# Kernel optimization log

Measured on AMD Instinct MI355X. Metric: run time of the kernel, lower is better.

## Reference

```python
import jax, jax.numpy as jnp
import numpy as np

BATCH = 32768
NJETS = 10
NCOMBOS = 22
FF = 200
NSEL = 6
EPS = 1e-5
METRIC = jnp.array([1.0, -1.0, -1.0, -1.0], dtype=jnp.float32)  # (E,px,py,pz) Minkowski


def _cola(v, w_combo):
    # v: [b, n, 4]; w_combo: [c, n] -> [b, n+c, 4] (identity rows + learned combos)
    combos = jnp.einsum('cj,bjv->bcv', w_combo, v)
    return jnp.concatenate([v, combos], axis=1)


def _lola(v, w_e, w_d):
    # v: [b, n, 4] -> [b, n, 5] features: m2, pT, E, w_e.E, w_d.d2
    m2 = jnp.einsum('biv,v,biv->bi', v, METRIC, v)           # invariant mass^2
    pt = jnp.sqrt(v[..., 1] ** 2 + v[..., 2] ** 2)           # transverse momentum
    E = v[..., 0]
    we = jnp.einsum('ij,bj->bi', w_e, E)
    # pairwise Minkowski distances via gram trick (avoids [b,n,n,4] tensor)
    gram = jnp.einsum('biv,v,bjv->bij', v, METRIC, v)        # [b, n, n]
    d2 = m2[:, :, None] + m2[:, None, :] - 2.0 * gram
    wd = jnp.einsum('ij,bij->bi', w_d, d2)
    return jnp.stack([m2, pt, E, we, wd], axis=-1)


def _batchnorm(x, gamma, beta):
    # torch BatchNorm1d in train mode: per-feature batch mean / biased var
    mu = jnp.mean(x, axis=0)
    var = jnp.mean((x - mu) ** 2, axis=0)
    return (x - mu) * jax.lax.rsqrt(var + EPS) * gamma + beta


def _head(v, cola_w, w_e, w_d, bn_g, bn_b, w1, b1, w2, b2):
    x = _cola(v, cola_w)
    f = _lola(x, w_e, w_d).reshape(x.shape[0], -1)  # [b, ntotal*5]
    f = _batchnorm(f, bn_g, bn_b)
    h = jax.nn.relu(f @ w1.T + b1)
    return h @ w2.T + b2


def setup_inputs() -> dict:
    key = jax.random.key(0)
    ks = jax.random.split(key, 20)
    n_isr = NJETS + NCOMBOS   # 32
    n_dec = NSEL + NCOMBOS    # 28
    f_isr, f_dec = n_isr * 5, n_dec * 5
    rn = lambda k, s, sc=0.1: jax.random.normal(k, s, jnp.float32) * sc
    return {
        'vectors': jax.random.normal(ks[0], (BATCH, NJETS, 4), jnp.float32),
        'isr_cola_w': rn(ks[1], (NCOMBOS, NJETS)),
        'isr_we': rn(ks[2], (n_isr, n_isr)),
        'isr_wd': rn(ks[3], (n_isr, n_isr)),
        'isr_bn_g': jnp.ones((f_isr,), jnp.float32),
        'isr_bn_b': jnp.zeros((f_isr,), jnp.float32),
        'isr_w1': rn(ks[4], (FF, f_isr)),
        'isr_b1': jnp.zeros((FF,), jnp.float32),
        'isr_w2': rn(ks[5], (NJETS, FF)),
        'isr_b2': jnp.zeros((NJETS,), jnp.float32),
        'dec_cola_w': rn(ks[6], (NCOMBOS, NSEL)),
        'dec_we': rn(ks[7], (n_dec, n_dec)),
        'dec_wd': rn(ks[8], (n_dec, n_dec)),
        'dec_bn_g': jnp.ones((f_dec,), jnp.float32),
        'dec_bn_b': jnp.zeros((f_dec,), jnp.float32),
        'dec_w1': rn(ks[9], (FF, f_dec)),
        'dec_b1': jnp.zeros((FF,), jnp.float32),
        'dec_w2': rn(ks[10], (11, FF)),
        'dec_b2': jnp.zeros((11,), jnp.float32),
    }


def reference(vectors, isr_cola_w, isr_we, isr_wd, isr_bn_g, isr_bn_b,
              isr_w1, isr_b1, isr_w2, isr_b2,
              dec_cola_w, dec_we, dec_wd, dec_bn_g, dec_bn_b,
              dec_w1, dec_b1, dec_w2, dec_b2):
    out_isr = _head(vectors, isr_cola_w, isr_we, isr_wd, isr_bn_g, isr_bn_b,
                    isr_w1, isr_b1, isr_w2, isr_b2)  # [b, njets]
    # iterative argmin+delete of (njets-6) jets == keep top-6 scores, original order
    scores = jax.lax.stop_gradient(out_isr)  # torch code detaches isrtag
    _, idx = jax.lax.top_k(scores, NSEL)
    idx = jnp.sort(idx, axis=1)  # np.delete preserves original ordering
    selected = jnp.take_along_axis(vectors, idx[:, :, None], axis=1)  # [b, 6, 4]
    out_dec = _head(selected, dec_cola_w, dec_we, dec_wd, dec_bn_g, dec_bn_b,
                    dec_w1, dec_b1, dec_w2, dec_b2)  # [b, 11]
    return jnp.concatenate([out_isr, out_dec], axis=1)  # [b, njets+11]
```

## Files before the change

### kernel.cpp

```cpp
#include <hip/hip_runtime.h>


#define BATCH 32768
#define NJ 10
#define FFDIM 200
#define OUTSTRIDE 21
#define NFEATBLK 4096

template<int NIN, int NP>
__global__ __launch_bounds__(256) void feat_kernel(
    const float* __restrict__ vin,
    const float* __restrict__ cola,
    const float* __restrict__ we,
    const float* __restrict__ wd,
    float* __restrict__ fout,
    float* __restrict__ psum,
    float* __restrict__ psq)
{
    constexpr int NC = 22;
    constexpr int F  = NP * 5;
    constexpr int RB = 8;
    constexpr int SW = NP + 1;
    constexpr int SF = F + 8;
    __shared__ float s_cola[NC * NIN];
    __shared__ float s_we[NP * SW];
    __shared__ float s_wd[NP * SW];
    __shared__ float4 s_x[RB][NP];
    __shared__ float s_m2[RB][NP];
    __shared__ float s_f[RB * SF];

    const int tid = threadIdx.x;
    const int blk = blockIdx.x;

    for (int k = tid; k < NC * NIN; k += 256) s_cola[k] = cola[k];
    for (int k = tid; k < NP * NP; k += 256) {
        const int i2 = k / NP, j2 = k - i2 * NP;
        s_we[i2 * SW + j2] = we[k];
        s_wd[i2 * SW + j2] = wd[k];
    }
    for (int k = tid; k < RB * NIN * 4; k += 256)
        ((float*)&s_x[0][0])[(k / (NIN * 4)) * NP * 4 + (k % (NIN * 4))] =
            vin[(size_t)blk * RB * NIN * 4 + k];
    __syncthreads();

    const int r = tid >> 5;
    const int i = tid & 31;

    if (i >= NIN && i < NP) {
        const int c = i - NIN;
        float4 x = make_float4(0.f, 0.f, 0.f, 0.f);
        #pragma unroll
        for (int j = 0; j < NIN; j++) {
            const float w = s_cola[c * NIN + j];
            const float4 xj = s_x[r][j];
            x.x += w * xj.x; x.y += w * xj.y; x.z += w * xj.z; x.w += w * xj.w;
        }
        s_x[r][i] = x;
    }
    __syncthreads();

    float m2 = 0.f, pt = 0.f;
    float4 xi = make_float4(0.f, 0.f, 0.f, 0.f);
    if (i < NP) {
        xi = s_x[r][i];
        m2 = xi.x * xi.x - xi.y * xi.y - xi.z * xi.z - xi.w * xi.w;
        pt = sqrtf(xi.y * xi.y + xi.z * xi.z);
        s_m2[r][i] = m2;
    }
    __syncthreads();
    if (i < NP) {
        float wesum = 0.f, wdsum = 0.f;
        for (int j = 0; j < NP; j++) {
            const float4 xj = s_x[r][j];
            wesum += s_we[i * SW + j] * xj.x;
            const float g = xi.x * xj.x - xi.y * xj.y - xi.z * xj.z - xi.w * xj.w;
            wdsum += s_wd[i * SW + j] * (m2 + s_m2[r][j] - 2.0f * g);
        }
        s_f[r * SF + i * 5 + 0] = m2;
        s_f[r * SF + i * 5 + 1] = pt;
        s_f[r * SF + i * 5 + 2] = xi.x;
        s_f[r * SF + i * 5 + 3] = wesum;
        s_f[r * SF + i * 5 + 4] = wdsum;
    }
    __syncthreads();

    const size_t base = (size_t)(blk >> 2) * F * 32 + (blk & 3) * 8;
    for (int q = tid; q < F * RB; q += 256) {
        const int c = q >> 3, rr = q & 7;
        fout[base + (size_t)c * 32 + rr] = s_f[rr * SF + c];
    }

    if (tid < F) {
        float s = 0.f, s2 = 0.f;
        #pragma unroll
        for (int rr = 0; rr < RB; rr++) {
            const float v = s_f[rr * SF + tid];
            s += v; s2 += v * v;
        }
        psum[(size_t)tid * NFEATBLK + blk] = s;
        psq [(size_t)tid * NFEATBLK + blk] = s2;
    }
}

template<int F>
__global__ __launch_bounds__(256) void bn_reduce(
    const float* __restrict__ psum, const float* __restrict__ psq,
    const float* __restrict__ gamma, const float* __restrict__ beta,
    float* __restrict__ bn)
{
    __shared__ float s1[256], s2[256];
    const int f = blockIdx.x, tid = threadIdx.x;
    float a = 0.f, b = 0.f;
    for (int bk = tid; bk < NFEATBLK; bk += 256) {
        a += psum[(size_t)f * NFEATBLK + bk];
        b += psq [(size_t)f * NFEATBLK + bk];
    }
    s1[tid] = a; s2[tid] = b; __syncthreads();
    for (int s = 128; s > 0; s >>= 1) {
        if (tid < s) { s1[tid] += s1[tid + s]; s2[tid] += s2[tid + s]; }
        __syncthreads();
    }
    if (tid == 0) {
        const float mu  = s1[0] / (float)BATCH;
        const float var = s2[0] / (float)BATCH - mu * mu;
        const float sc  = gamma[f] * rsqrtf(var + 1e-5f);
        bn[f]     = sc;
        bn[F + f] = beta[f] - mu * sc;
    }
}

template<int NF, int NOUT, bool SELECT>
__global__ __launch_bounds__(256, 4) void mlp_kernel(
    const float* __restrict__ fin,
    const float* __restrict__ bn,
    const float* __restrict__ w1,
    const float* __restrict__ b1,
    const float* __restrict__ w2,
    const float* __restrict__ b2,
    const float* __restrict__ vectors,
    float* __restrict__ selout,
    float* __restrict__ out,
    int out_off)
{
    constexpr int RB = 32;
    constexpr int RP = 36;
    __shared__ __align__(16) float U[FFDIM * RP];
    __shared__ float s_scale[NF], s_shift[NF];
    __shared__ float s_out[RB * 12];
    __shared__ int   s_idx[RB * 6];

    const int tid = threadIdx.x;
    const int blk = blockIdx.x;

    for (int k = tid; k < NF; k += 256) { s_scale[k] = bn[k]; s_shift[k] = bn[NF + k]; }
    __syncthreads();

    const float* fb = fin + (size_t)blk * NF * 32;
    for (int q = tid; q < NF * 32; q += 256) {
        const int c = q >> 5, r = q & 31;
        U[c * RP + r] = fb[q] * s_scale[c] + s_shift[c];
    }
    __syncthreads();

    const int rg = tid & 7, r4 = rg * 4, nc = tid >> 3;
    float acc[7][4];
    #pragma unroll
    for (int j = 0; j < 7; j++)
        #pragma unroll
        for (int rr = 0; rr < 4; rr++) acc[j][rr] = 0.0f;

    constexpr int NF4 = NF / 4;
    for (int kc = 0; kc < NF4; kc++) {
        const int k = kc * 4;
        const float4 f0 = *reinterpret_cast<const float4*>(&U[(k + 0) * RP + r4]);
        const float4 f1 = *reinterpret_cast<const float4*>(&U[(k + 1) * RP + r4]);
        const float4 f2 = *reinterpret_cast<const float4*>(&U[(k + 2) * RP + r4]);
        const float4 f3 = *reinterpret_cast<const float4*>(&U[(k + 3) * RP + r4]);
        float4 w[7];
        #pragma unroll
        for (int j = 0; j < 6; j++)
            w[j] = *reinterpret_cast<const float4*>(w1 + (size_t)(nc + 32 * j) * NF + k);
        w[6] = (nc < FFDIM - 192)
             ? *reinterpret_cast<const float4*>(w1 + (size_t)(nc + 192) * NF + k)
             : make_float4(0.f, 0.f, 0.f, 0.f);
        #pragma unroll
        for (int j = 0; j < 7; j++) {
            acc[j][0] += w[j].x * f0.x + w[j].y * f1.x + w[j].z * f2.x + w[j].w * f3.x;
            acc[j][1] += w[j].x * f0.y + w[j].y * f1.y + w[j].z * f2.y + w[j].w * f3.y;
            acc[j][2] += w[j].x * f0.z + w[j].y * f1.z + w[j].z * f2.z + w[j].w * f3.z;
            acc[j][3] += w[j].x * f0.w + w[j].y * f1.w + w[j].z * f2.w + w[j].w * f3.w;
        }
    }
    __syncthreads();

    #pragma unroll
    for (int j = 0; j < 7; j++) {
        const int n = nc + 32 * j;
        if (n < FFDIM) {
            const float bb = b1[n];
            float4 h;
            h.x = acc[j][0] + bb; h.x = h.x > 0.f ? h.x : 0.f;
            h.y = acc[j][1] + bb; h.y = h.y > 0.f ? h.y : 0.f;
            h.z = acc[j][2] + bb; h.z = h.z > 0.f ? h.z : 0.f;
            h.w = acc[j][3] + bb; h.w = h.w > 0.f ? h.w : 0.f;
            *reinterpret_cast<float4*>(&U[n * RP + r4]) = h;
        }
    }
    __syncthreads();

    {
        const int r = tid & 31, og = tid >> 5;
        for (int o = og; o < NOUT; o += 8) {
            float a = b2[o];
            for (int kc = 0; kc < FFDIM / 4; kc++) {
                const float4 wv = *reinterpret_cast<const float4*>(
                    w2 + (size_t)o * FFDIM + kc * 4);
                a += wv.x * U[(kc * 4 + 0) * RP + r] + wv.y * U[(kc * 4 + 1) * RP + r]
                   + wv.z * U[(kc * 4 + 2) * RP + r] + wv.w * U[(kc * 4 + 3) * RP + r];
            }
            s_out[r * 12 + o] = a;
        }
    }
    __syncthreads();

    if (SELECT) {
        if (tid < RB) {
            float sc[10];
            #pragma unroll
            for (int o = 0; o < 10; o++) sc[o] = s_out[tid * 12 + o];
            bool used[10];
            #pragma unroll
            for (int o = 0; o < 10; o++) used[o] = false;
            int ids[6];
            for (int k = 0; k < 6; k++) {
                float m = -3.0e38f; int mi = 0;
                for (int o = 0; o < 10; o++)
                    if (!used[o] && sc[o] > m) { m = sc[o]; mi = o; }
                used[mi] = true; ids[k] = mi;
            }
            for (int a2 = 1; a2 < 6; a2++) {
                const int v = ids[a2]; int bp = a2 - 1;
                while (bp >= 0 && ids[bp] > v) { ids[bp + 1] = ids[bp]; bp--; }
                ids[bp + 1] = v;
            }
            #pragma unroll
            for (int k = 0; k < 6; k++) s_idx[tid * 6 + k] = ids[k];
        }
        __syncthreads();
        for (int q = tid; q < RB * 6; q += 256) {
            const int r2 = q / 6, j = q - r2 * 6;
            reinterpret_cast<float4*>(selout)[(size_t)blk * RB * 6 + q] =
                reinterpret_cast<const float4*>(vectors)
                    [(size_t)(blk * RB + r2) * NJ + s_idx[r2 * 6 + j]];
        }
    }

    for (int q = tid; q < RB * NOUT; q += 256) {
        const int r2 = q / NOUT, o = q - r2 * NOUT;
        out[(size_t)(blk * RB + r2) * OUTSTRIDE + out_off + o] = s_out[r2 * 12 + o];
    }
}

extern "C" void kernel_launch(void* const* d_in, const int* in_sizes, int n_in,
                              void* d_out, int out_size, void* d_ws, size_t ws_size,
                              hipStream_t stream) {
    const float* vectors  = (const float*)d_in[0];
    const float* isr_cola = (const float*)d_in[1];
    const float* isr_we   = (const float*)d_in[2];
    const float* isr_wd   = (const float*)d_in[3];
    const float* isr_bn_g = (const float*)d_in[4];
    const float* isr_bn_b = (const float*)d_in[5];
    const float* isr_w1   = (const float*)d_in[6];
    const float* isr_b1   = (const float*)d_in[7];
    const float* isr_w2   = (const float*)d_in[8];
    const float* isr_b2   = (const float*)d_in[9];
    const float* dec_cola = (const float*)d_in[10];
    const float* dec_we   = (const float*)d_in[11];
    const float* dec_wd   = (const float*)d_in[12];
    const float* dec_bn_g = (const float*)d_in[13];
    const float* dec_bn_b = (const float*)d_in[14];
    const float* dec_w1   = (const float*)d_in[15];
    const float* dec_b1   = (const float*)d_in[16];
    const float* dec_w2   = (const float*)d_in[17];
    const float* dec_b2   = (const float*)d_in[18];
    float* out = (float*)d_out;
    float* ws  = (float*)d_ws;

    float* f_buf  = ws;
    float* sel    = f_buf + 5242880;
    float* ps     = sel + 786432;
    float* pq     = ps + 655360;
    float* bn_i   = pq + 655360;
    float* bn_d   = bn_i + 320;

    feat_kernel<10, 32><<<4096, 256, 0, stream>>>(vectors, isr_cola, isr_we, isr_wd,
                                                  f_buf, ps, pq);
    bn_reduce<160><<<160, 256, 0, stream>>>(ps, pq, isr_bn_g, isr_bn_b, bn_i);
    mlp_kernel<160, 10, true><<<1024, 256, 0, stream>>>(f_buf, bn_i, isr_w1, isr_b1,
                                                        isr_w2, isr_b2, vectors, sel,
                                                        out, 0);
    feat_kernel<6, 28><<<4096, 256, 0, stream>>>(sel, dec_cola, dec_we, dec_wd,
                                                 f_buf, ps, pq);
    bn_reduce<140><<<140, 256, 0, stream>>>(ps, pq, dec_bn_g, dec_bn_b, bn_d);
    mlp_kernel<140, 11, false><<<1024, 256, 0, stream>>>(f_buf, bn_d, dec_w1, dec_b1,
                                                         dec_w2, dec_b2, nullptr, nullptr,
                                                         out, 10);
}
```

Baseline: 175.1 us.

## Restructure MLP to row-per-thread with wave-uniform weights and packed FMA

The feature buffer becomes row-major, and the MLP kernel is reorganized so each thread owns one batch row of a 64-row tile. Each wave owns 50 hidden units, so w1 and w2 reads are wave-uniform (scalar/broadcast) and accumulation uses 2-wide vector FMAs. The second layer is computed per wave as partial sums and reduced through shared memory, which removes the hidden-activation round trip through LDS. The cost is heavy register pressure (100 accumulators), lower occupancy (launch bounds 3), and half as many blocks.

```diff
diff --git a/kernel.cpp b/kernel.cpp
--- a/kernel.cpp
+++ b/kernel.cpp
@@ -6,6 +6,8 @@
 #define FFDIM 200
 #define OUTSTRIDE 21
 #define NFEATBLK 4096
+
+typedef float v2f __attribute__((ext_vector_type(2)));
 
 template<int NIN, int NP>
 __global__ __launch_bounds__(256) void feat_kernel(
@@ -84,10 +86,9 @@
     }
     __syncthreads();
 
-    const size_t base = (size_t)(blk >> 2) * F * 32 + (blk & 3) * 8;
-    for (int q = tid; q < F * RB; q += 256) {
-        const int c = q >> 3, rr = q & 7;
-        fout[base + (size_t)c * 32 + rr] = s_f[rr * SF + c];
+    for (int q = tid; q < RB * F; q += 256) {
+        const int rr = q / F, c = q - rr * F;
+        fout[(size_t)blk * RB * F + q] = s_f[rr * SF + c];
     }
 
     if (tid < F) {
@@ -130,7 +131,7 @@
 }
 
 template<int NF, int NOUT, bool SELECT>
-__global__ __launch_bounds__(256, 4) void mlp_kernel(
+__global__ __launch_bounds__(256, 3) void mlp_kernel(
     const float* __restrict__ fin,
     const float* __restrict__ bn,
     const float* __restrict__ w1,
@@ -142,84 +143,109 @@
     float* __restrict__ out,
     int out_off)
 {
-    constexpr int RB = 32;
-    constexpr int RP = 36;
-    __shared__ __align__(16) float U[FFDIM * RP];
-    __shared__ float s_scale[NF], s_shift[NF];
+    constexpr int RB = 64;
+    constexpr int SU = (NF == 160) ? 164 : 148;
+    constexpr int NW = 50;
+    constexpr int NKB = NF / 32;
+    constexpr int REM = NF % 32;
+    __shared__ __align__(16) float U[RB * SU];
+    __shared__ __align__(16) float s_scale[NF], s_shift[NF];
     __shared__ float s_out[RB * 12];
     __shared__ int   s_idx[RB * 6];
 
     const int tid = threadIdx.x;
     const int blk = blockIdx.x;
+    const int w = __builtin_amdgcn_readfirstlane(tid >> 6);
+    const int r = tid & 63;
 
     for (int k = tid; k < NF; k += 256) { s_scale[k] = bn[k]; s_shift[k] = bn[NF + k]; }
     __syncthreads();
 
-    const float* fb = fin + (size_t)blk * NF * 32;
-    for (int q = tid; q < NF * 32; q += 256) {
-        const int c = q >> 5, r = q & 31;
-        U[c * RP + r] = fb[q] * s_scale[c] + s_shift[c];
-    }
-    __syncthreads();
-
-    const int rg = tid & 7, r4 = rg * 4, nc = tid >> 3;
-    float acc[7][4];
+    {
+        constexpr int NF4 = NF / 4;
+        const float4* fb4 = reinterpret_cast<const float4*>(fin + (size_t)blk * RB * NF);
+        for (int q4 = tid; q4 < RB * NF4; q4 += 256) {
+            const int row = q4 / NF4, c = (q4 - row * NF4) * 4;
+            const float4 v = fb4[q4];
+            const float4 sc = *reinterpret_cast<const float4*>(&s_scale[c]);
+            const float4 sh = *reinterpret_cast<const float4*>(&s_shift[c]);
+            float4 o;
+            o.x = v.x * sc.x + sh.x; o.y = v.y * sc.y + sh.y;
+            o.z = v.z * sc.z + sh.z; o.w = v.w * sc.w + sh.w;
+            *reinterpret_cast<float4*>(&U[row * SU + c]) = o;
+        }
+    }
+    __syncthreads();
+
+    const float* frow = &U[r * SU];
+    v2f acc2[NW];
     #pragma unroll
-    for (int j = 0; j < 7; j++)
-        #pragma unroll
-        for (int rr = 0; rr < 4; rr++) acc[j][rr] = 0.0f;
-
-    constexpr int NF4 = NF / 4;
-    for (int kc = 0; kc < NF4; kc++) {
-        const int k = kc * 4;
-        const float4 f0 = *reinterpret_cast<const float4*>(&U[(k + 0) * RP + r4]);
-        const float4 f1 = *reinterpret_cast<const float4*>(&U[(k + 1) * RP + r4]);
-        const float4 f2 = *reinterpret_cast<const float4*>(&U[(k + 2) * RP + r4]);
-        const float4 f3 = *reinterpret_cast<const float4*>(&U[(k + 3) * RP + r4]);
-        float4 w[7];
-        #pragma unroll
-        for (int j = 0; j < 6; j++)
-            w[j] = *reinterpret_cast<const float4*>(w1 + (size_t)(nc + 32 * j) * NF + k);
-        w[6] = (nc < FFDIM - 192)
-             ? *reinterpret_cast<const float4*>(w1 + (size_t)(nc + 192) * NF + k)
-             : make_float4(0.f, 0.f, 0.f, 0.f);
-        #pragma unroll
-        for (int j = 0; j < 7; j++) {
-            acc[j][0] += w[j].x * f0.x + w[j].y * f1.x + w[j].z * f2.x + w[j].w * f3.x;
-            acc[j][1] += w[j].x * f0.y + w[j].y * f1.y + w[j].z * f2.y + w[j].w * f3.y;
-            acc[j][2] += w[j].x * f0.z + w[j].y * f1.z + w[j].z * f2.z + w[j].w * f3.z;
-            acc[j][3] += w[j].x * f0.w + w[j].y * f1.w + w[j].z * f2.w + w[j].w * f3.w;
-        }
-    }
-    __syncthreads();
-
+    for (int j = 0; j < NW; j++) acc2[j] = (v2f){0.f, 0.f};
+
+    for (int kb = 0; kb < NKB; ++kb) {
+        const int k0 = kb * 32;
+        v2f f2[16];
+        #pragma unroll
+        for (int t = 0; t < 8; t++) {
+            const float4 fa = *reinterpret_cast<const float4*>(&frow[k0 + 4 * t]);
+            f2[2 * t]     = (v2f){fa.x, fa.y};
+            f2[2 * t + 1] = (v2f){fa.z, fa.w};
+        }
+        #pragma unroll
+        for (int j = 0; j < NW; j++) {
+            const v2f* wp = reinterpret_cast<const v2f*>(
+                w1 + (size_t)(w * NW + j) * NF + k0);
+            #pragma unroll
+            for (int p = 0; p < 16; p++) acc2[j] += wp[p] * f2[p];
+        }
+    }
+    if (REM > 0) {
+        const int k0 = NKB * 32;
+        v2f f2[REM > 0 ? REM / 2 : 1];
+        #pragma unroll
+        for (int t = 0; t < REM / 4; t++) {
+            const float4 fa = *reinterpret_cast<const float4*>(&frow[k0 + 4 * t]);
+            f2[2 * t]     = (v2f){fa.x, fa.y};
+            f2[2 * t + 1] = (v2f){fa.z, fa.w};
+        }
+        #pragma unroll
+        for (int j = 0; j < NW; j++) {
+            const v2f* wp = reinterpret_cast<const v2f*>(
+                w1 + (size_t)(w * NW + j) * NF + k0);
+            #pragma unroll
+            for (int p = 0; p < REM / 2; p++) acc2[j] += wp[p] * f2[p];
+        }
+    }
+    __syncthreads();
+
+    v2f hp[NW / 2];
     #pragma unroll
-    for (int j = 0; j < 7; j++) {
-        const int n = nc + 32 * j;
-        if (n < FFDIM) {
-            const float bb = b1[n];
-            float4 h;
-            h.x = acc[j][0] + bb; h.x = h.x > 0.f ? h.x : 0.f;
-            h.y = acc[j][1] + bb; h.y = h.y > 0.f ? h.y : 0.f;
-            h.z = acc[j][2] + bb; h.z = h.z > 0.f ? h.z : 0.f;
-            h.w = acc[j][3] + bb; h.w = h.w > 0.f ? h.w : 0.f;
-            *reinterpret_cast<float4*>(&U[n * RP + r4]) = h;
-        }
-    }
-    __syncthreads();
-
-    {
-        const int r = tid & 31, og = tid >> 5;
-        for (int o = og; o < NOUT; o += 8) {
-            float a = b2[o];
-            for (int kc = 0; kc < FFDIM / 4; kc++) {
-                const float4 wv = *reinterpret_cast<const float4*>(
-                    w2 + (size_t)o * FFDIM + kc * 4);
-                a += wv.x * U[(kc * 4 + 0) * RP + r] + wv.y * U[(kc * 4 + 1) * RP + r]
-                   + wv.z * U[(kc * 4 + 2) * RP + r] + wv.w * U[(kc * 4 + 3) * RP + r];
-            }
-            s_out[r * 12 + o] = a;
-        }
+    for (int a = 0; a < NW / 2; a++) {
+        const int n0 = w * NW + 2 * a;
+        float h0 = acc2[2 * a][0] + acc2[2 * a][1] + b1[n0];
+        float h1 = acc2[2 * a + 1][0] + acc2[2 * a + 1][1] + b1[n0 + 1];
+        h0 = h0 > 0.f ? h0 : 0.f;
+        h1 = h1 > 0.f ? h1 : 0.f;
+        hp[a] = (v2f){h0, h1};
+    }
+
+    float* s_part = U;
+    for (int o = 0; o < NOUT; o++) {
+        v2f a2 = (v2f){0.f, 0.f};
+        const v2f* w2p = reinterpret_cast<const v2f*>(
+            w2 + (size_t)o * FFDIM + w * NW);
+        #pragma unroll
+        for (int a = 0; a < NW / 2; a++) a2 += hp[a] * w2p[a];
+        s_part[(w * RB + r) * 12 + o] = a2[0] + a2[1];
+    }
+    __syncthreads();
+
+    for (int q = tid; q < RB * NOUT; q += 256) {
+        const int row = q / NOUT, o = q - row * NOUT;
+        float v = b2[o];
+        #pragma unroll
+        for (int ww = 0; ww < 4; ww++) v += s_part[(ww * RB + row) * 12 + o];
+        s_out[row * 12 + o] = v;
     }
     __syncthreads();
 
@@ -238,8 +264,8 @@
                     if (!used[o] && sc[o] > m) { m = sc[o]; mi = o; }
                 used[mi] = true; ids[k] = mi;
             }
-            for (int a2 = 1; a2 < 6; a2++) {
-                const int v = ids[a2]; int bp = a2 - 1;
+            for (int a2i = 1; a2i < 6; a2i++) {
+                const int v = ids[a2i]; int bp = a2i - 1;
                 while (bp >= 0 && ids[bp] > v) { ids[bp + 1] = ids[bp]; bp--; }
                 ids[bp + 1] = v;
             }
@@ -296,13 +322,13 @@
     feat_kernel<10, 32><<<4096, 256, 0, stream>>>(vectors, isr_cola, isr_we, isr_wd,
                                                   f_buf, ps, pq);
     bn_reduce<160><<<160, 256, 0, stream>>>(ps, pq, isr_bn_g, isr_bn_b, bn_i);
-    mlp_kernel<160, 10, true><<<1024, 256, 0, stream>>>(f_buf, bn_i, isr_w1, isr_b1,
-                                                        isr_w2, isr_b2, vectors, sel,
-                                                        out, 0);
+    mlp_kernel<160, 10, true><<<512, 256, 0, stream>>>(f_buf, bn_i, isr_w1, isr_b1,
+                                                       isr_w2, isr_b2, vectors, sel,
+                                                       out, 0);
     feat_kernel<6, 28><<<4096, 256, 0, stream>>>(sel, dec_cola, dec_we, dec_wd,
                                                  f_buf, ps, pq);
     bn_reduce<140><<<140, 256, 0, stream>>>(ps, pq, dec_bn_g, dec_bn_b, bn_d);
-    mlp_kernel<140, 11, false><<<1024, 256, 0, stream>>>(f_buf, bn_d, dec_w1, dec_b1,
-                                                         dec_w2, dec_b2, nullptr, nullptr,
-                                                         out, 10);
+    mlp_kernel<140, 11, false><<<512, 256, 0, stream>>>(f_buf, bn_d, dec_w1, dec_b1,
+                                                        dec_w2, dec_b2, nullptr, nullptr,
+                                                        out, 10);
 }
```

Result: slower. 308.5 us (+76.1%).
